# Performance work log

Hardware: AMD Instinct MI355X
Metric: run time of the kernel (lower is better)

## Reference

```python
import jax, jax.numpy as jnp
import numpy as np

B, T, DP, A = 1024, 256, 64, 8   # batch, num particles (seq len), particle dim, action dim
H = 256                          # recurr_size (GRU hidden)
HID = 256                        # MLP hidden
C = 2                            # num_critics
TIME_NORM = 100.0


def setup_inputs() -> dict:
    key = jax.random.key(0)
    ks = jax.random.split(key, 10)
    F = DP + 1        # features + weight channel
    DIN = H + A + 1   # encoding + action + time
    s = lambda k, shape: (jax.random.normal(k, shape, jnp.float32) * 0.05)
    return {
        "particles": jax.random.normal(ks[0], (B, T, DP), jnp.float32),
        "weights": jax.random.uniform(ks[1], (B, T), jnp.float32),
        "action": jax.random.normal(ks[2], (B, A), jnp.float32),
        "time_idx": jax.random.uniform(ks[3], (B,), jnp.float32) * TIME_NORM,
        # GRU params (flax GRUCell layout, gates fused as [r|z|n]):
        "Wi": s(ks[4], (F, 3 * H)),    # input kernel (ir|iz|in), with bias
        "bi": jnp.zeros((3 * H,), jnp.float32),
        "Wh": s(ks[5], (H, 3 * H)),    # hidden kernel (hr|hz|hn); only hn has bias
        "bhn": jnp.zeros((H,), jnp.float32),
        # Two MLPDecoder critics stacked on leading dim C:
        "W1": s(ks[6], (C, DIN, HID)),
        "b1": jnp.zeros((C, HID), jnp.float32),
        "W2": s(ks[7], (C, HID, HID)),
        "b2": jnp.zeros((C, HID), jnp.float32),
        "W3": s(ks[8], (C, HID, 1)),
        "b3": jnp.zeros((C, 1), jnp.float32),
    }


def reference(particles, weights, action, time_idx, Wi, bi, Wh, bhn, W1, b1, W2, b2, W3, b3):
    # feature_fn = identity; append particle weights as an extra channel
    inputs = jnp.concatenate([particles, weights[..., None]], axis=-1)  # [B,T,F]
    # Precompute all input projections (parallel over time), scan only the recurrence.
    xp = jnp.einsum('btf,fg->btg', inputs, Wi) + bi                     # [B,T,3H]
    xp = jnp.swapaxes(xp, 0, 1)                                         # [T,B,3H]
    h0 = jnp.zeros((inputs.shape[0], H), inputs.dtype)

    def step(h, x):
        hp = h @ Wh                                                     # [B,3H]
        r = jax.nn.sigmoid(x[:, :H] + hp[:, :H])
        z = jax.nn.sigmoid(x[:, H:2 * H] + hp[:, H:2 * H])
        n = jnp.tanh(x[:, 2 * H:] + r * (hp[:, 2 * H:] + bhn))
        h_new = (1.0 - z) * n + z * h
        return h_new, None

    h, _ = jax.lax.scan(step, h0, xp)                                   # last encoding [B,H]

    t = (time_idx / TIME_NORM)[:, None]                                 # [B,1]
    x = jnp.concatenate([h, action, t], axis=-1)                        # [B,DIN]

    # Both critic MLPs batched over leading critic dim C (ReLU hidden layers).
    h1 = jax.nn.relu(jnp.einsum('bd,cdh->cbh', x, W1) + b1[:, None, :])   # [C,B,HID]
    h2 = jax.nn.relu(jnp.einsum('cbh,chk->cbk', h1, W2) + b2[:, None, :]) # [C,B,HID]
    v = jnp.einsum('cbh,cho->cbo', h2, W3) + b3[:, None, :]               # [C,B,1]
    return jnp.moveaxis(v[..., 0], 0, -1)                               # [B,C]
```

## Files before the change

kernel.cpp:

```cpp
#include <hip/hip_runtime.h>


#define TSEQ 256
#define DPDIM 64

typedef float f32x4 __attribute__((ext_vector_type(4)));
typedef __bf16 bf16x8 __attribute__((ext_vector_type(8)));
typedef unsigned short ushort8 __attribute__((ext_vector_type(8)));

static __device__ __forceinline__ unsigned short f2bf(float f) {
  unsigned u = __builtin_bit_cast(unsigned, f);
  return (unsigned short)((u + 0x7fffu + ((u >> 16) & 1u)) >> 16);
}
static __device__ __forceinline__ float bf2f(unsigned short h) {
  return __builtin_bit_cast(float, ((unsigned)h) << 16);
}
static __device__ __forceinline__ float sigm(float x) {
  return __builtin_amdgcn_rcpf(1.f + __expf(-x));
}
static __device__ __forceinline__ float tanh_fast(float p) {
  float q = __expf(-2.f * fabsf(p));
  float t = (1.f - q) * __builtin_amdgcn_rcpf(1.f + q);
  return __builtin_bit_cast(float, __builtin_bit_cast(unsigned, t) |
                                   (__builtin_bit_cast(unsigned, p) & 0x80000000u));
}

#define OFF_WIT 0
#define OFF_XP  110592
#define OFF_H0  135168
#define OFF_H1  137888
#define OFF_BI  140608
#define OFF_W64 143680
#define LDS_GRU 146752

#define HSTRIDE 544

__global__ __launch_bounds__(512, 2) void gru_kernel(
    const float* __restrict__ particles, const float* __restrict__ weights,
    const float* __restrict__ Wi, const float* __restrict__ bi,
    const float* __restrict__ Wh, const float* __restrict__ bhn,
    unsigned short* __restrict__ hT)
{
  extern __shared__ char smem[];
  const int tid  = threadIdx.x;
  const int lane = tid & 63;
  const int w    = tid >> 6;
  const int l15  = lane & 15;
  const int kg   = lane >> 4;
  const int b0   = blockIdx.x * 4;

  for (int idx = tid; idx < 64 * 768; idx += 512) {
    int k = idx / 768, n = idx - k * 768;
    *(unsigned short*)(smem + OFF_WIT + n * 144 + k * 2) = f2bf(Wi[idx]);
  }
  for (int idx = tid; idx < 768; idx += 512) {
    *(float*)(smem + OFF_BI  + idx * 4) = bi[idx];
    *(float*)(smem + OFF_W64 + idx * 4) = Wi[64 * 768 + idx];
  }
  for (int idx = tid; idx < (2 * 5 * HSTRIDE) / 4; idx += 512)
    ((unsigned*)(smem + OFF_H0))[idx] = 0u;

  const int hcol0 = w * 16 + l15;
  const float bhn0 = bhn[hcol0];
  const float bhn1 = bhn[hcol0 + 128];

  bf16x8 whb[6][8];
  #pragma unroll
  for (int j = 0; j < 6; ++j) {
    const int tile = w + 8 * j;
    const float* wp = Wh + (size_t)(kg * 8) * 768 + tile * 16 + l15;
    #pragma unroll
    for (int ks = 0; ks < 8; ++ks) {
      ushort8 tmp;
      #pragma unroll
      for (int e = 0; e < 8; ++e)
        tmp[e] = f2bf(wp[(size_t)(ks * 32 + e) * 768]);
      whb[j][ks] = __builtin_bit_cast(bf16x8, tmp);
    }
  }
  __syncthreads();

  const unsigned arow = ((l15 & 3) == 0)
                      ? (unsigned)((l15 >> 2) * HSTRIDE + kg * 16)
                      : (unsigned)(4 * HSTRIDE + kg * 16);

  const float* pbase = particles +
      ((size_t)(b0 + (l15 >> 2)) * TSEQ + (l15 & 3)) * DPDIM + kg * 8;
  const float* wbase = weights + (size_t)(b0 + kg) * TSEQ;

  char* const xpb = smem + OFF_XP + hcol0 * 8 + kg * 2;

  f32x4 acc[6];
  const f32x4 fzero = {0.f, 0.f, 0.f, 0.f};
  float hreg0 = 0.f, hreg1 = 0.f;

  for (int g = 0; g < 64; ++g) {
    const int t0 = g * 4;

    #pragma unroll
    for (int j = 0; j < 6; ++j) acc[j] = fzero;
    #pragma unroll
    for (int ks = 0; ks < 2; ++ks) {
      const float* pp = pbase + (size_t)t0 * DPDIM + ks * 32;
      f32x4 pa = *(const f32x4*)pp;
      f32x4 pb = *(const f32x4*)(pp + 4);
      ushort8 tmp;
      tmp[0] = f2bf(pa[0]); tmp[1] = f2bf(pa[1]); tmp[2] = f2bf(pa[2]); tmp[3] = f2bf(pa[3]);
      tmp[4] = f2bf(pb[0]); tmp[5] = f2bf(pb[1]); tmp[6] = f2bf(pb[2]); tmp[7] = f2bf(pb[3]);
      bf16x8 af = __builtin_bit_cast(bf16x8, tmp);
      #pragma unroll
      for (int j = 0; j < 6; ++j) {
        const int n = hcol0 + 128 * j;
        bf16x8 bf = *(const bf16x8*)(smem + OFF_WIT + n * 144 + ks * 64 + kg * 16);
        acc[j] = __builtin_amdgcn_mfma_f32_16x16x32_bf16(af, bf, acc[j], 0, 0, 0);
      }
    }
    {
      f32x4 wv = *(const f32x4*)(wbase + t0);
      #pragma unroll
      for (int j = 0; j < 6; ++j) {
        const int col = hcol0 + 128 * j;
        const float biv  = *(const float*)(smem + OFF_BI  + col * 4);
        const float w64v = *(const float*)(smem + OFF_W64 + col * 4);
        #pragma unroll
        for (int r = 0; r < 4; ++r)
          *(unsigned short*)(xpb + j * 4096 + r * 1024) =
              f2bf(acc[j][r] + biv + wv[r] * w64v);
      }
    }

    #pragma unroll
    for (int tt = 0; tt < 4; ++tt) {
      const int t     = t0 + tt;
      const int rboff = (t & 1) ? OFF_H1 : OFF_H0;
      const int wboff = (t & 1) ? OFF_H0 : OFF_H1;
      #pragma unroll
      for (int j = 0; j < 6; ++j) acc[j] = fzero;
      const char* hb = smem + rboff;
      #pragma unroll
      for (int ks = 0; ks < 8; ++ks) {
        bf16x8 af = *(const bf16x8*)(hb + arow + ks * 64);
        #pragma unroll
        for (int j = 0; j < 6; ++j)
          acc[j] = __builtin_amdgcn_mfma_f32_16x16x32_bf16(af, whb[j][ks], acc[j], 0, 0, 0);
      }
      float xr0 = bf2f(*(const unsigned short*)(xpb + 0 * 4096 + tt * 1024));
      float xr1 = bf2f(*(const unsigned short*)(xpb + 1 * 4096 + tt * 1024));
      float xz0 = bf2f(*(const unsigned short*)(xpb + 2 * 4096 + tt * 1024));
      float xz1 = bf2f(*(const unsigned short*)(xpb + 3 * 4096 + tt * 1024));
      float xn0 = bf2f(*(const unsigned short*)(xpb + 4 * 4096 + tt * 1024));
      float xn1 = bf2f(*(const unsigned short*)(xpb + 5 * 4096 + tt * 1024));
      float rr0 = sigm(xr0 + acc[0][0]);
      float zz0 = sigm(xz0 + acc[2][0]);
      float nn0 = tanh_fast(xn0 + rr0 * (acc[4][0] + bhn0));
      unsigned short h0u = f2bf(nn0 + zz0 * (hreg0 - nn0));
      hreg0 = bf2f(h0u);
      float rr1 = sigm(xr1 + acc[1][0]);
      float zz1 = sigm(xz1 + acc[3][0]);
      float nn1 = tanh_fast(xn1 + rr1 * (acc[5][0] + bhn1));
      unsigned short h1u = f2bf(nn1 + zz1 * (hreg1 - nn1));
      hreg1 = bf2f(h1u);
      *(unsigned short*)(smem + wboff + kg * HSTRIDE + hcol0 * 2)         = h0u;
      *(unsigned short*)(smem + wboff + kg * HSTRIDE + (hcol0 + 128) * 2) = h1u;
      __syncthreads();
    }
  }

  hT[(size_t)(b0 + kg) * 256 + hcol0]       = f2bf(hreg0);
  hT[(size_t)(b0 + kg) * 256 + hcol0 + 128] = f2bf(hreg1);
}

#define HOFF_XA 0
#define HOFF_B  37888
#define HOFF_H1 58368
#define HOFF_H2 92160
#define HOFF_B1 125952
#define HOFF_B2 126976
#define HOFF_W3 128000
#define LDS_HEAD 129024

#define HROWS 32

__global__ __launch_bounds__(512) void head_kernel(
    const unsigned short* __restrict__ hT, const float* __restrict__ action,
    const float* __restrict__ time_idx, const float* __restrict__ W1,
    const float* __restrict__ b1, const float* __restrict__ W2,
    const float* __restrict__ b2, const float* __restrict__ W3,
    const float* __restrict__ b3, float* __restrict__ out)
{
  extern __shared__ char smem[];
  const int tid  = threadIdx.x;
  const int lane = tid & 63;
  const int w    = tid >> 6;
  const int l15  = lane & 15;
  const int kg   = lane >> 4;
  const int c    = blockIdx.x & 1;
  const int rt   = blockIdx.x >> 1;
  const int r0   = rt * HROWS;

  if (tid < 256) {
    *(float*)(smem + HOFF_B1 + tid * 4) = b1[c * 256 + tid];
    *(float*)(smem + HOFF_B2 + tid * 4) = b2[c * 256 + tid];
    *(float*)(smem + HOFF_W3 + tid * 4) = W3[c * 256 + tid];
  }
  for (int idx = tid; idx < HROWS * 296; idx += 512) {
    int row = idx / 296, k = idx - row * 296;
    unsigned short v;
    if (k < 256)       v = hT[(r0 + row) * 256 + k];
    else if (k < 264)  v = f2bf(action[(r0 + row) * 8 + (k - 256)]);
    else if (k == 264) v = f2bf(time_idx[r0 + row] * 0.01f);
    else               v = 0;
    *(unsigned short*)(smem + HOFF_XA + row * 592 + k * 2) = v;
  }

  f32x4 acc[2][2];
  const f32x4 fzero = {0.f, 0.f, 0.f, 0.f};

  #pragma unroll
  for (int mt = 0; mt < 2; ++mt)
    #pragma unroll
    for (int i = 0; i < 2; ++i) acc[mt][i] = fzero;
  for (int ks = 0; ks < 9; ++ks) {
    for (int idx = tid; idx < 32 * 256; idx += 512) {
      int kk = idx >> 8, n = idx & 255;
      int kglob = ks * 32 + kk;
      float v = (kglob < 265) ? W1[((size_t)c * 265 + kglob) * 256 + n] : 0.f;
      *(unsigned short*)(smem + HOFF_B + n * 80 + kk * 2) = f2bf(v);
    }
    __syncthreads();
    bf16x8 bfr[2];
    #pragma unroll
    for (int i = 0; i < 2; ++i)
      bfr[i] = *(const bf16x8*)(smem + HOFF_B + ((w * 2 + i) * 16 + l15) * 80 + kg * 16);
    #pragma unroll
    for (int mt = 0; mt < 2; ++mt) {
      bf16x8 af = *(const bf16x8*)(smem + HOFF_XA + (mt * 16 + l15) * 592 + ks * 64 + kg * 16);
      #pragma unroll
      for (int i = 0; i < 2; ++i)
        acc[mt][i] = __builtin_amdgcn_mfma_f32_16x16x32_bf16(af, bfr[i], acc[mt][i], 0, 0, 0);
    }
    __syncthreads();
  }
  #pragma unroll
  for (int mt = 0; mt < 2; ++mt)
    #pragma unroll
    for (int i = 0; i < 2; ++i) {
      int col = (w * 2 + i) * 16 + l15;
      float bv = *(const float*)(smem + HOFF_B1 + col * 4);
      #pragma unroll
      for (int r = 0; r < 4; ++r) {
        float v = acc[mt][i][r] + bv; v = v > 0.f ? v : 0.f;
        *(unsigned short*)(smem + HOFF_H1 + (mt * 16 + kg * 4 + r) * 528 + col * 2) = f2bf(v);
      }
    }
  __syncthreads();

  #pragma unroll
  for (int mt = 0; mt < 2; ++mt)
    #pragma unroll
    for (int i = 0; i < 2; ++i) acc[mt][i] = fzero;
  for (int ks = 0; ks < 8; ++ks) {
    for (int idx = tid; idx < 32 * 256; idx += 512) {
      int kk = idx >> 8, n = idx & 255;
      float v = W2[((size_t)c * 256 + ks * 32 + kk) * 256 + n];
      *(unsigned short*)(smem + HOFF_B + n * 80 + kk * 2) = f2bf(v);
    }
    __syncthreads();
    bf16x8 bfr[2];
    #pragma unroll
    for (int i = 0; i < 2; ++i)
      bfr[i] = *(const bf16x8*)(smem + HOFF_B + ((w * 2 + i) * 16 + l15) * 80 + kg * 16);
    #pragma unroll
    for (int mt = 0; mt < 2; ++mt) {
      bf16x8 af = *(const bf16x8*)(smem + HOFF_H1 + (mt * 16 + l15) * 528 + ks * 64 + kg * 16);
      #pragma unroll
      for (int i = 0; i < 2; ++i)
        acc[mt][i] = __builtin_amdgcn_mfma_f32_16x16x32_bf16(af, bfr[i], acc[mt][i], 0, 0, 0);
    }
    __syncthreads();
  }
  #pragma unroll
  for (int mt = 0; mt < 2; ++mt)
    #pragma unroll
    for (int i = 0; i < 2; ++i) {
      int col = (w * 2 + i) * 16 + l15;
      float bv = *(const float*)(smem + HOFF_B2 + col * 4);
      #pragma unroll
      for (int r = 0; r < 4; ++r) {
        float v = acc[mt][i][r] + bv; v = v > 0.f ? v : 0.f;
        *(unsigned short*)(smem + HOFF_H2 + (mt * 16 + kg * 4 + r) * 528 + col * 2) = f2bf(v);
      }
    }
  __syncthreads();

  {
    int row = tid >> 2, q = tid & 3;
    if (row < HROWS) {
      float s = 0.f;
      #pragma unroll
      for (int i = 0; i < 16; ++i) {
        uint2 hh = *(const uint2*)(smem + HOFF_H2 + row * 528 + (q * 64 + i * 4) * 2);
        const float* w3p = (const float*)(smem + HOFF_W3) + q * 64 + i * 4;
        s += bf2f((unsigned short)hh.x)         * w3p[0];
        s += bf2f((unsigned short)(hh.x >> 16)) * w3p[1];
        s += bf2f((unsigned short)hh.y)         * w3p[2];
        s += bf2f((unsigned short)(hh.y >> 16)) * w3p[3];
      }
      s += __shfl_xor(s, 1);
      s += __shfl_xor(s, 2);
      if (q == 0) out[(r0 + row) * 2 + c] = s + b3[c];
    }
  }
}

extern "C" void kernel_launch(void* const* d_in, const int* in_sizes, int n_in,
                              void* d_out, int out_size, void* d_ws, size_t ws_size,
                              hipStream_t stream) {
  const float* particles = (const float*)d_in[0];
  const float* weights   = (const float*)d_in[1];
  const float* action    = (const float*)d_in[2];
  const float* time_idx  = (const float*)d_in[3];
  const float* Wi        = (const float*)d_in[4];
  const float* bi        = (const float*)d_in[5];
  const float* Wh        = (const float*)d_in[6];
  const float* bhn       = (const float*)d_in[7];
  const float* W1        = (const float*)d_in[8];
  const float* b1        = (const float*)d_in[9];
  const float* W2        = (const float*)d_in[10];
  const float* b2        = (const float*)d_in[11];
  const float* W3        = (const float*)d_in[12];
  const float* b3        = (const float*)d_in[13];
  unsigned short* hT = (unsigned short*)d_ws;
  float* out = (float*)d_out;

  (void)hipFuncSetAttribute((const void*)gru_kernel,
                            hipFuncAttributeMaxDynamicSharedMemorySize, LDS_GRU);
  (void)hipFuncSetAttribute((const void*)head_kernel,
                            hipFuncAttributeMaxDynamicSharedMemorySize, LDS_HEAD);

  hipLaunchKernelGGL(gru_kernel, dim3(256), dim3(512), LDS_GRU, stream,
                     particles, weights, Wi, bi, Wh, bhn, hT);
  hipLaunchKernelGGL(head_kernel, dim3(64), dim3(512), LDS_HEAD, stream,
                     hT, action, time_idx, W1, b1, W2, b2, W3, b3, out);
}
```

Measured before the change: 712.0 us.

## Stage full critic weight matrices in LDS once and drop per-k-step syncs

The head kernel now converts the whole W1 and W2 for a critic into LDS in one pass with vectorized float4 loads, replacing nine and eight k-step tiles that each needed two barriers. Hidden-state A fragments are read straight from global memory, and the action/time tail is built in registers. LDS regions are overlapped and usage rises to about 158KB, which forces one block per CU. The head runs after the long GRU recurrence kernel, so this change only affects a small part of total time.

```diff
diff --git a/kernel.cpp b/kernel.cpp
--- a/kernel.cpp
+++ b/kernel.cpp
@@ -170,18 +170,19 @@
   hT[(size_t)(b0 + kg) * 256 + hcol0 + 128] = f2bf(hreg1);
 }
 
-#define HOFF_XA 0
-#define HOFF_B  37888
-#define HOFF_H1 58368
-#define HOFF_H2 92160
-#define HOFF_B1 125952
-#define HOFF_B2 126976
-#define HOFF_W3 128000
-#define LDS_HEAD 129024
+#define HOFF_W1 0
+#define HOFF_WT 135168
+#define HOFF_H1 0
+#define HOFF_W2 16896
+#define HOFF_H2 135168
+#define HOFF_B1 155648
+#define HOFF_B2 156672
+#define HOFF_W3 157696
+#define LDS_HEAD 158720
 
 #define HROWS 32
 
-__global__ __launch_bounds__(512) void head_kernel(
+__global__ __launch_bounds__(512, 1) void head_kernel(
     const unsigned short* __restrict__ hT, const float* __restrict__ action,
     const float* __restrict__ time_idx, const float* __restrict__ W1,
     const float* __restrict__ b1, const float* __restrict__ W2,
@@ -203,15 +204,41 @@
     *(float*)(smem + HOFF_B2 + tid * 4) = b2[c * 256 + tid];
     *(float*)(smem + HOFF_W3 + tid * 4) = W3[c * 256 + tid];
   }
-  for (int idx = tid; idx < HROWS * 296; idx += 512) {
-    int row = idx / 296, k = idx - row * 296;
-    unsigned short v;
-    if (k < 256)       v = hT[(r0 + row) * 256 + k];
-    else if (k < 264)  v = f2bf(action[(r0 + row) * 8 + (k - 256)]);
-    else if (k == 264) v = f2bf(time_idx[r0 + row] * 0.01f);
-    else               v = 0;
-    *(unsigned short*)(smem + HOFF_XA + row * 592 + k * 2) = v;
-  }
+  for (int idx = tid; idx < 20480 / 4; idx += 512)
+    ((unsigned*)(smem + HOFF_WT))[idx] = 0u;
+  __syncthreads();
+
+  for (int q = tid; q < 64 * 256; q += 512) {
+    int k = q >> 6, n0 = (q & 63) * 4;
+    f32x4 v = *(const f32x4*)(W1 + ((size_t)c * 265 + k) * 256 + n0);
+    char* d = smem + HOFF_W1 + k * 2;
+    *(unsigned short*)(d + (size_t)(n0 + 0) * 528) = f2bf(v[0]);
+    *(unsigned short*)(d + (size_t)(n0 + 1) * 528) = f2bf(v[1]);
+    *(unsigned short*)(d + (size_t)(n0 + 2) * 528) = f2bf(v[2]);
+    *(unsigned short*)(d + (size_t)(n0 + 3) * 528) = f2bf(v[3]);
+  }
+  for (int idx = tid; idx < 9 * 256; idx += 512) {
+    int kk = idx >> 8, n = idx & 255;
+    *(unsigned short*)(smem + HOFF_WT + n * 80 + kk * 2) =
+        f2bf(W1[((size_t)c * 265 + 256 + kk) * 256 + n]);
+  }
+
+  ushort8 atail[2];
+  #pragma unroll
+  for (int mt = 0; mt < 2; ++mt) {
+    int row = r0 + mt * 16 + l15;
+    ushort8 t8 = {0, 0, 0, 0, 0, 0, 0, 0};
+    if (kg == 0) {
+      f32x4 a0 = *(const f32x4*)(action + (size_t)row * 8);
+      f32x4 a1 = *(const f32x4*)(action + (size_t)row * 8 + 4);
+      t8[0] = f2bf(a0[0]); t8[1] = f2bf(a0[1]); t8[2] = f2bf(a0[2]); t8[3] = f2bf(a0[3]);
+      t8[4] = f2bf(a1[0]); t8[5] = f2bf(a1[1]); t8[6] = f2bf(a1[2]); t8[7] = f2bf(a1[3]);
+    } else if (kg == 1) {
+      t8[0] = f2bf(time_idx[row] * 0.01f);
+    }
+    atail[mt] = t8;
+  }
+  __syncthreads();
 
   f32x4 acc[2][2];
   const f32x4 fzero = {0.f, 0.f, 0.f, 0.f};
@@ -220,27 +247,29 @@
   for (int mt = 0; mt < 2; ++mt)
     #pragma unroll
     for (int i = 0; i < 2; ++i) acc[mt][i] = fzero;
-  for (int ks = 0; ks < 9; ++ks) {
-    for (int idx = tid; idx < 32 * 256; idx += 512) {
-      int kk = idx >> 8, n = idx & 255;
-      int kglob = ks * 32 + kk;
-      float v = (kglob < 265) ? W1[((size_t)c * 265 + kglob) * 256 + n] : 0.f;
-      *(unsigned short*)(smem + HOFF_B + n * 80 + kk * 2) = f2bf(v);
-    }
-    __syncthreads();
-    bf16x8 bfr[2];
-    #pragma unroll
-    for (int i = 0; i < 2; ++i)
-      bfr[i] = *(const bf16x8*)(smem + HOFF_B + ((w * 2 + i) * 16 + l15) * 80 + kg * 16);
+  #pragma unroll
+  for (int ks = 0; ks < 8; ++ks) {
+    bf16x8 bfr0 = *(const bf16x8*)(smem + HOFF_W1 + ((w * 2 + 0) * 16 + l15) * 528 + ks * 64 + kg * 16);
+    bf16x8 bfr1 = *(const bf16x8*)(smem + HOFF_W1 + ((w * 2 + 1) * 16 + l15) * 528 + ks * 64 + kg * 16);
     #pragma unroll
     for (int mt = 0; mt < 2; ++mt) {
-      bf16x8 af = *(const bf16x8*)(smem + HOFF_XA + (mt * 16 + l15) * 592 + ks * 64 + kg * 16);
-      #pragma unroll
-      for (int i = 0; i < 2; ++i)
-        acc[mt][i] = __builtin_amdgcn_mfma_f32_16x16x32_bf16(af, bfr[i], acc[mt][i], 0, 0, 0);
-    }
-    __syncthreads();
-  }
+      bf16x8 af = *(const bf16x8*)(hT + (size_t)(r0 + mt * 16 + l15) * 256 + ks * 32 + kg * 8);
+      acc[mt][0] = __builtin_amdgcn_mfma_f32_16x16x32_bf16(af, bfr0, acc[mt][0], 0, 0, 0);
+      acc[mt][1] = __builtin_amdgcn_mfma_f32_16x16x32_bf16(af, bfr1, acc[mt][1], 0, 0, 0);
+    }
+  }
+  {
+    bf16x8 bfr0 = *(const bf16x8*)(smem + HOFF_WT + ((w * 2 + 0) * 16 + l15) * 80 + kg * 16);
+    bf16x8 bfr1 = *(const bf16x8*)(smem + HOFF_WT + ((w * 2 + 1) * 16 + l15) * 80 + kg * 16);
+    #pragma unroll
+    for (int mt = 0; mt < 2; ++mt) {
+      bf16x8 af = __builtin_bit_cast(bf16x8, atail[mt]);
+      acc[mt][0] = __builtin_amdgcn_mfma_f32_16x16x32_bf16(af, bfr0, acc[mt][0], 0, 0, 0);
+      acc[mt][1] = __builtin_amdgcn_mfma_f32_16x16x32_bf16(af, bfr1, acc[mt][1], 0, 0, 0);
+    }
+  }
+  __syncthreads();
+
   #pragma unroll
   for (int mt = 0; mt < 2; ++mt)
     #pragma unroll
@@ -253,32 +282,34 @@
         *(unsigned short*)(smem + HOFF_H1 + (mt * 16 + kg * 4 + r) * 528 + col * 2) = f2bf(v);
       }
     }
+  for (int q = tid; q < 64 * 256; q += 512) {
+    int k = q >> 6, n0 = (q & 63) * 4;
+    f32x4 v = *(const f32x4*)(W2 + ((size_t)c * 256 + k) * 256 + n0);
+    char* d = smem + HOFF_W2 + k * 2;
+    *(unsigned short*)(d + (size_t)(n0 + 0) * 528) = f2bf(v[0]);
+    *(unsigned short*)(d + (size_t)(n0 + 1) * 528) = f2bf(v[1]);
+    *(unsigned short*)(d + (size_t)(n0 + 2) * 528) = f2bf(v[2]);
+    *(unsigned short*)(d + (size_t)(n0 + 3) * 528) = f2bf(v[3]);
+  }
   __syncthreads();
 
   #pragma unroll
   for (int mt = 0; mt < 2; ++mt)
     #pragma unroll
     for (int i = 0; i < 2; ++i) acc[mt][i] = fzero;
+  #pragma unroll
   for (int ks = 0; ks < 8; ++ks) {
-    for (int idx = tid; idx < 32 * 256; idx += 512) {
-      int kk = idx >> 8, n = idx & 255;
-      float v = W2[((size_t)c * 256 + ks * 32 + kk) * 256 + n];
-      *(unsigned short*)(smem + HOFF_B + n * 80 + kk * 2) = f2bf(v);
-    }
-    __syncthreads();
-    bf16x8 bfr[2];
-    #pragma unroll
-    for (int i = 0; i < 2; ++i)
-      bfr[i] = *(const bf16x8*)(smem + HOFF_B + ((w * 2 + i) * 16 + l15) * 80 + kg * 16);
+    bf16x8 bfr0 = *(const bf16x8*)(smem + HOFF_W2 + ((w * 2 + 0) * 16 + l15) * 528 + ks * 64 + kg * 16);
+    bf16x8 bfr1 = *(const bf16x8*)(smem + HOFF_W2 + ((w * 2 + 1) * 16 + l15) * 528 + ks * 64 + kg * 16);
     #pragma unroll
     for (int mt = 0; mt < 2; ++mt) {
       bf16x8 af = *(const bf16x8*)(smem + HOFF_H1 + (mt * 16 + l15) * 528 + ks * 64 + kg * 16);
-      #pragma unroll
-      for (int i = 0; i < 2; ++i)
-        acc[mt][i] = __builtin_amdgcn_mfma_f32_16x16x32_bf16(af, bfr[i], acc[mt][i], 0, 0, 0);
-    }
-    __syncthreads();
-  }
+      acc[mt][0] = __builtin_amdgcn_mfma_f32_16x16x32_bf16(af, bfr0, acc[mt][0], 0, 0, 0);
+      acc[mt][1] = __builtin_amdgcn_mfma_f32_16x16x32_bf16(af, bfr1, acc[mt][1], 0, 0, 0);
+    }
+  }
+  __syncthreads();
+
   #pragma unroll
   for (int mt = 0; mt < 2; ++mt)
     #pragma unroll
```

New measurement: 713.4 us. No clear change (+0.2%).
